# Kernel tuning notes

Hardware: AMD Instinct MI355X
Metric: run time of the kernel (lower is better)

The kernel has to match this reference:

```python
import jax, jax.numpy as jnp
import numpy as np

B, C, H, W = 1, 64, 448, 608
S1, S2 = 32, 16  # stage_1_classes, stage_2_classes


def _leaky(v):
    # F.leaky_relu default negative_slope=0.01
    return jnp.where(v >= 0, v, 0.01 * v)


def setup_inputs() -> dict:
    key = jax.random.key(0)
    ks = jax.random.split(key, 7)
    x = jax.random.normal(ks[0], (B, C, H, W), jnp.float32)
    w1 = jax.random.normal(ks[1], (H, S1, C), jnp.float32) * 0.05
    b1 = jax.random.normal(ks[2], (H, S1), jnp.float32) * 0.05
    # stage_2: CondMul(H*S1, C, S2)
    w2 = jax.random.normal(ks[3], (H * S1, C, S2), jnp.float32) * 0.05
    b2 = jax.random.normal(ks[4], (H * S1, S2), jnp.float32) * 0.05
    w3 = jax.random.normal(ks[5], (H * S1 * S2, C, 2), jnp.float32) * 0.02
    b3 = jax.random.normal(ks[6], (H * S1 * S2, 2), jnp.float32) * 0.02
    return {"x": x, "w1": w1, "b1": b1, "w2": w2, "b2": b2, "w3": w3, "b3": b3}


def reference(x, w1, b1, w2, b2, w3, b3):
    b = x.shape[0]
    # stage 1: grouped 1x1 conv == per-row GEMM over channels
    classes1 = _leaky(jnp.einsum('bchw,hkc->bhkw', x, w1) + b1[None, :, :, None])  # (B,H,S1,W)
    inds1 = jnp.argmax(classes1, axis=2)  # (B,H,W)
    inds = inds1 + jnp.arange(H)[None, :, None] * S1  # global row-offset index
    # flatten pixels: (B,H,W,C) -> (N,C)
    x2 = jnp.transpose(x, (0, 2, 3, 1)).reshape(-1, C)  # (N,C), N=B*H*W
    inds = inds.reshape(-1)  # (N,)
    # stage 2: CondMul gather -> per-pixel (C x S2) matvec
    classes2 = _leaky(jnp.einsum('nc,nck->nk', x2, w2[inds]) + b2[inds])  # (N,S2)
    inds2 = inds * S2 + jnp.argmax(classes2, axis=1)  # (N,)
    reg = jnp.einsum('nc,nck->nk', x2, w3[inds2]) + b3[inds2]  # (N,2)
    x_2 = jnp.transpose(reg.reshape(b, H, W, 2), (0, 3, 1, 2))  # (B,2,H,W)
    offset = jnp.arange(H)[None, None, :, None]  # (1,1,H,1)
    inds_loc = inds2.reshape(b, 1, H, W) - offset * S1 * S2  # local class in [0, S1*S2)
    scale = (1.0 / S1) * S2  # matches torch operator precedence: (1.0/S1)*S2 = 0.5
    x_out = (inds_loc.astype(jnp.float32) + x_2[:, 0, :, :]) * scale  # (B,1,H,W) for B=1
    mask = _leaky(x_2[:, 1, :, :])  # (B,H,W)
    return x_out, mask
```

## Files before the change

### kernel.cpp

```cpp
#include <hip/hip_runtime.h>

#define HH 448
#define WW 608
#define CC 64
#define S1 32
#define S2 16
#define HW (HH * WW)
#define BLK 640
#define W2N (S1 * CC * S2)
#define W2N4 (W2N / 4)
#define NSTG 13


__launch_bounds__(BLK, 3)
__global__ void reg2stage_kernel(const float* __restrict__ x,
                                 const float* __restrict__ w1,
                                 const float* __restrict__ b1,
                                 const float* __restrict__ w2,
                                 const float* __restrict__ b2,
                                 const float* __restrict__ w3,
                                 const float* __restrict__ b3,
                                 float* __restrict__ out) {
    __shared__ float w2s[W2N];
    __shared__ float b2s[S1 * S2];

    const int h = blockIdx.x;
    const int tid = threadIdx.x;
    const int w = tid;
    const bool active = (w < WW);

    float xv[CC];
    if (active) {
        const float* __restrict__ xp = x + (size_t)h * WW + w;
#pragma unroll
        for (int c = 0; c < CC; ++c) xv[c] = xp[(size_t)c * HW];
    }

    const float4* __restrict__ w2row4 =
        reinterpret_cast<const float4*>(w2 + (size_t)h * W2N);
    float4 stg[NSTG];
#pragma unroll
    for (int i = 0; i < NSTG; ++i) {
        const int e4 = tid + i * BLK;
        if (e4 < W2N4) stg[i] = w2row4[e4];
    }
    float b2v = 0.0f;
    if (tid < S1 * S2) b2v = b2[(size_t)h * (S1 * S2) + tid];

    const float* __restrict__ w1r = w1 + (size_t)h * (S1 * CC);
    const float* __restrict__ b1r = b1 + (size_t)h * S1;
    float best1 = -INFINITY;
    int k1 = 0;
    if (active) {
        for (int k = 0; k < S1; ++k) {
            float acc = b1r[k];
            const float* __restrict__ wk = w1r + k * CC;
#pragma unroll
            for (int c = 0; c < CC; ++c) acc += xv[c] * wk[c];
            if (acc > best1) { best1 = acc; k1 = k; }
        }
    }

#pragma unroll
    for (int i = 0; i < NSTG; ++i) {
        const int e4 = tid + i * BLK;
        if (e4 < W2N4) {
            const int e = e4 * 4;
            const int k = e >> 10;
            const int c = (e >> 4) & 63;
            const int k2b = e & 15;
            const int cx = c ^ ((k & 15) << 2);
            const float vv[4] = {stg[i].x, stg[i].y, stg[i].z, stg[i].w};
#pragma unroll
            for (int j = 0; j < 4; ++j)
                w2s[k * 1024 + (k2b + j) * 64 + cx] = vv[j];
        }
    }
    if (tid < S1 * S2) {
        const int k = tid >> 4, k2 = tid & 15;
        b2s[k2 * 32 + k] = b2v;
    }
    __syncthreads();

    if (!active) return;

    float acc2[S2];
#pragma unroll
    for (int k2 = 0; k2 < S2; ++k2) acc2[k2] = b2s[k2 * 32 + k1];

    const int cxor = (k1 & 15) << 2;
    const float4* __restrict__ w2s4 = reinterpret_cast<const float4*>(w2s);
#pragma unroll
    for (int c4 = 0; c4 < 16; ++c4) {
        const float x0 = xv[4 * c4], x1 = xv[4 * c4 + 1];
        const float x2 = xv[4 * c4 + 2], x3 = xv[4 * c4 + 3];
        const int cg = (4 * c4) ^ cxor;
#pragma unroll
        for (int k2 = 0; k2 < S2; ++k2) {
            const float4 q = w2s4[(k1 * 1024 + k2 * 64 + cg) >> 2];
            acc2[k2] += x0 * q.x + x1 * q.y + x2 * q.z + x3 * q.w;
        }
    }
    float best2 = -INFINITY;
    int k2b = 0;
#pragma unroll
    for (int k2 = 0; k2 < S2; ++k2) {
        if (acc2[k2] > best2) { best2 = acc2[k2]; k2b = k2; }
    }

    const size_t ind2 = ((size_t)h * S1 + k1) * S2 + k2b;
    const float4* __restrict__ w3p =
        reinterpret_cast<const float4*>(w3 + ind2 * (CC * 2));
    float r0 = b3[ind2 * 2];
    float r1 = b3[ind2 * 2 + 1];
#pragma unroll
    for (int j = 0; j < 32; ++j) {
        const float4 q = w3p[j];
        r0 += xv[2 * j] * q.x + xv[2 * j + 1] * q.z;
        r1 += xv[2 * j] * q.y + xv[2 * j + 1] * q.w;
    }

    const int loc = k1 * S2 + k2b;
    const float x_out = ((float)loc + r0) * 0.5f;
    const float mask = (r1 >= 0.0f) ? r1 : 0.01f * r1;

    out[(size_t)h * WW + w] = x_out;
    out[(size_t)HW + (size_t)h * WW + w] = mask;
}

extern "C" void kernel_launch(void* const* d_in, const int* in_sizes, int n_in,
                              void* d_out, int out_size, void* d_ws, size_t ws_size,
                              hipStream_t stream) {
    const float* x  = (const float*)d_in[0];
    const float* w1 = (const float*)d_in[1];
    const float* b1 = (const float*)d_in[2];
    const float* w2 = (const float*)d_in[3];
    const float* b2 = (const float*)d_in[4];
    const float* w3 = (const float*)d_in[5];
    const float* b3 = (const float*)d_in[6];
    float* out = (float*)d_out;

    reg2stage_kernel<<<dim3(HH), dim3(BLK), 0, stream>>>(x, w1, b1, w2, b2, w3, b3, out);
}
```

Measured before the change: 84.54 us.

## Stage w2 into LDS via direct global_load_lds in two channel halves

Replaces the register-staged transpose of the per-row w2 slab with direct global-to-LDS loads (global_load_lds) and a new swizzled layout. The slab is split into two channel halves, so LDS holds only half at a time, and the stage-2 matvec runs in two passes with extra barriers between them. This halves shared memory and removes the staging registers, allowing launch bounds of 5 blocks per CU instead of 3. The cost is a second barrier round trip, and the second half's load is serialized after the first half's compute.

```diff
diff --git a/kernel.cpp b/kernel.cpp
--- a/kernel.cpp
+++ b/kernel.cpp
@@ -7,12 +7,27 @@
 #define S2 16
 #define HW (HH * WW)
 #define BLK 640
-#define W2N (S1 * CC * S2)
-#define W2N4 (W2N / 4)
-#define NSTG 13
+#define NCH 4096
 
+typedef __attribute__((address_space(1))) const void* gp1_t;
+typedef __attribute__((address_space(3))) void* lp3_t;
 
-__launch_bounds__(BLK, 3)
+__device__ __forceinline__ void stage_chunk(const float* __restrict__ w2row,
+                                            float* w2s_base, int i, int hf) {
+    const int k   = i >> 7;
+    const int r   = i & 127;
+    const int clx = r >> 2;
+    const int q2x = r & 3;
+    const int cl  = clx ^ ((k >> 2) & 1);
+    const int c   = hf * 32 + cl;
+    const int k2q = q2x ^ (k & 3);
+    const int g   = ((k << 6) + c) * 4 + k2q;
+    __builtin_amdgcn_global_load_lds((gp1_t)(w2row + (size_t)g * 4),
+                                     (lp3_t)(w2s_base + (size_t)i * 4),
+                                     16, 0, 0);
+}
+
+__launch_bounds__(BLK, 5)
 __global__ void reg2stage_kernel(const float* __restrict__ x,
                                  const float* __restrict__ w1,
                                  const float* __restrict__ b1,
@@ -21,13 +36,22 @@
                                  const float* __restrict__ w3,
                                  const float* __restrict__ b3,
                                  float* __restrict__ out) {
-    __shared__ float w2s[W2N];
+    __shared__ float w2s[S1 * 32 * S2];
     __shared__ float b2s[S1 * S2];
 
     const int h = blockIdx.x;
     const int tid = threadIdx.x;
+    const bool active = (tid < WW);
     const int w = tid;
-    const bool active = (w < WW);
+
+    const float* __restrict__ w2row = w2 + (size_t)h * (S1 * CC * S2);
+
+#pragma unroll
+    for (int j = 0; j < 6; ++j) stage_chunk(w2row, w2s, tid + j * BLK, 0);
+    if (tid < NCH - 6 * BLK) stage_chunk(w2row, w2s, 6 * BLK + tid, 0);
+
+    float b2v = 0.0f;
+    if (tid < S1 * S2) b2v = b2[(size_t)h * (S1 * S2) + tid];
 
     float xv[CC];
     if (active) {
@@ -35,17 +59,6 @@
 #pragma unroll
         for (int c = 0; c < CC; ++c) xv[c] = xp[(size_t)c * HW];
     }
-
-    const float4* __restrict__ w2row4 =
-        reinterpret_cast<const float4*>(w2 + (size_t)h * W2N);
-    float4 stg[NSTG];
-#pragma unroll
-    for (int i = 0; i < NSTG; ++i) {
-        const int e4 = tid + i * BLK;
-        if (e4 < W2N4) stg[i] = w2row4[e4];
-    }
-    float b2v = 0.0f;
-    if (tid < S1 * S2) b2v = b2[(size_t)h * (S1 * S2) + tid];
 
     const float* __restrict__ w1r = w1 + (size_t)h * (S1 * CC);
     const float* __restrict__ b1r = b1 + (size_t)h * S1;
@@ -61,46 +74,58 @@
         }
     }
 
-#pragma unroll
-    for (int i = 0; i < NSTG; ++i) {
-        const int e4 = tid + i * BLK;
-        if (e4 < W2N4) {
-            const int e = e4 * 4;
-            const int k = e >> 10;
-            const int c = (e >> 4) & 63;
-            const int k2b = e & 15;
-            const int cx = c ^ ((k & 15) << 2);
-            const float vv[4] = {stg[i].x, stg[i].y, stg[i].z, stg[i].w};
-#pragma unroll
-            for (int j = 0; j < 4; ++j)
-                w2s[k * 1024 + (k2b + j) * 64 + cx] = vv[j];
-        }
-    }
     if (tid < S1 * S2) {
         const int k = tid >> 4, k2 = tid & 15;
         b2s[k2 * 32 + k] = b2v;
     }
     __syncthreads();
 
+    float acc2[S2];
+    const int kbase = k1 << 9;
+    const int clxor = (k1 >> 2) & 1;
+    const int q2xor = k1 & 3;
+    if (active) {
+#pragma unroll
+        for (int t = 0; t < S2; ++t) acc2[t] = b2s[t * 32 + k1];
+#pragma unroll 8
+        for (int cl = 0; cl < 32; ++cl) {
+            const float xc = xv[cl];
+            const int rowb = kbase + ((cl ^ clxor) << 4);
+#pragma unroll
+            for (int q = 0; q < 4; ++q) {
+                const float4 v = *reinterpret_cast<const float4*>(
+                    &w2s[rowb + ((q ^ q2xor) << 2)]);
+                acc2[4 * q + 0] += xc * v.x;
+                acc2[4 * q + 1] += xc * v.y;
+                acc2[4 * q + 2] += xc * v.z;
+                acc2[4 * q + 3] += xc * v.w;
+            }
+        }
+    }
+    __syncthreads();
+
+#pragma unroll
+    for (int j = 0; j < 6; ++j) stage_chunk(w2row, w2s, tid + j * BLK, 1);
+    if (tid < NCH - 6 * BLK) stage_chunk(w2row, w2s, 6 * BLK + tid, 1);
+    __syncthreads();
+
     if (!active) return;
 
-    float acc2[S2];
+#pragma unroll 8
+    for (int cl = 0; cl < 32; ++cl) {
+        const float xc = xv[32 + cl];
+        const int rowb = kbase + ((cl ^ clxor) << 4);
 #pragma unroll
-    for (int k2 = 0; k2 < S2; ++k2) acc2[k2] = b2s[k2 * 32 + k1];
-
-    const int cxor = (k1 & 15) << 2;
-    const float4* __restrict__ w2s4 = reinterpret_cast<const float4*>(w2s);
-#pragma unroll
-    for (int c4 = 0; c4 < 16; ++c4) {
-        const float x0 = xv[4 * c4], x1 = xv[4 * c4 + 1];
-        const float x2 = xv[4 * c4 + 2], x3 = xv[4 * c4 + 3];
-        const int cg = (4 * c4) ^ cxor;
-#pragma unroll
-        for (int k2 = 0; k2 < S2; ++k2) {
-            const float4 q = w2s4[(k1 * 1024 + k2 * 64 + cg) >> 2];
-            acc2[k2] += x0 * q.x + x1 * q.y + x2 * q.z + x3 * q.w;
+        for (int q = 0; q < 4; ++q) {
+            const float4 v = *reinterpret_cast<const float4*>(
+                &w2s[rowb + ((q ^ q2xor) << 2)]);
+            acc2[4 * q + 0] += xc * v.x;
+            acc2[4 * q + 1] += xc * v.y;
+            acc2[4 * q + 2] += xc * v.z;
+            acc2[4 * q + 3] += xc * v.w;
         }
     }
+
     float best2 = -INFINITY;
     int k2b = 0;
 #pragma unroll
```

Result: slower. 213.1 us (+152.1%).
